# Kernel optimization log

Hardware: AMD Instinct MI355X
Metric: run time of the kernel (lower is better)

The kernel has to match this reference:

```python
import jax, jax.numpy as jnp
import numpy as np

B, N, D, H = 4, 2048, 256, 4
DH = D // H
SS = DH ** -0.25  # sqrt(scale), applied to both qk0 and qk1
EPS = 1e-5


def _split_heads(t):
    # [B, N, D] -> [B, H, N, DH]
    b, n, _ = t.shape
    return t.reshape(b, n, H, DH).transpose(0, 2, 1, 3)


def _merge_heads(t):
    # [B, H, N, DH] -> [B, N, D]
    b, h, n, dh = t.shape
    return t.transpose(0, 2, 1, 3).reshape(b, n, h * dh)


def _layernorm(x, g, b):
    mu = jnp.mean(x, axis=-1, keepdims=True)
    var = jnp.mean(jnp.square(x - mu), axis=-1, keepdims=True)
    return (x - mu) * jax.lax.rsqrt(var + EPS) * g + b


def setup_inputs() -> dict:
    key = jax.random.key(0)
    ks = jax.random.split(key, 16)
    s = 0.02
    return {
        "x0": jax.random.normal(ks[0], (B, N, D), jnp.float32),
        "x1": jax.random.normal(ks[1], (B, N, D), jnp.float32),
        # weights stored as [in, out] (y = x @ W + b), matching torch Linear math
        "Wqk": jax.random.normal(ks[2], (D, D), jnp.float32) * s,
        "bqk": jnp.zeros((D,), jnp.float32),
        "Wv": jax.random.normal(ks[3], (D, D), jnp.float32) * s,
        "bv": jnp.zeros((D,), jnp.float32),
        "Wo": jax.random.normal(ks[4], (D, D), jnp.float32) * s,
        "bo": jnp.zeros((D,), jnp.float32),
        "W1": jax.random.normal(ks[5], (2 * D, 2 * D), jnp.float32) * s,
        "b1": jnp.zeros((2 * D,), jnp.float32),
        "ln_g": jnp.ones((2 * D,), jnp.float32),
        "ln_b": jnp.zeros((2 * D,), jnp.float32),
        "W2": jax.random.normal(ks[6], (2 * D, D), jnp.float32) * s,
        "b2": jnp.zeros((D,), jnp.float32),
    }


def reference(x0, x1, Wqk, bqk, Wv, bv, Wo, bo, W1, b1, ln_g, ln_b, W2, b2):
    qk0 = _split_heads(x0 @ Wqk + bqk) * SS  # [B,H,N,DH]
    qk1 = _split_heads(x1 @ Wqk + bqk) * SS
    v0 = _split_heads(x0 @ Wv + bv)
    v1 = _split_heads(x1 @ Wv + bv)

    # single shared similarity matrix, reused for both softmax directions
    sim = jnp.einsum("bhid,bhjd->bhij", qk0, qk1)  # [B,H,N0,N1]
    attn01 = jax.nn.softmax(sim, axis=-1)                      # rows over j
    attn10 = jax.nn.softmax(jnp.swapaxes(sim, -1, -2), axis=-1)  # rows over i

    m0 = jnp.einsum("bhij,bhjd->bhid", attn01, v1)  # [B,H,N0,DH]
    m1 = jnp.einsum("bhji,bhjd->bhid", jnp.swapaxes(attn10, -1, -2), v0)

    m0 = _merge_heads(m0) @ Wo + bo  # [B,N,D]
    m1 = _merge_heads(m1) @ Wo + bo

    def ffn(x, m):
        h = jnp.concatenate([x, m], axis=-1) @ W1 + b1
        h = jax.nn.gelu(_layernorm(h, ln_g, ln_b), approximate=False)
        return x + h @ W2 + b2

    return ffn(x0, m0), ffn(x1, m1)
```

## Files before the change

### kernel.cpp

```cpp
#include <hip/hip_runtime.h>
#include <hip/hip_bf16.h>
#include <math.h>

#define DEV static __device__ __forceinline__

typedef float f32x4 __attribute__((ext_vector_type(4)));
typedef short s16x8 __attribute__((ext_vector_type(8)));
typedef unsigned short u16;
typedef unsigned int u32;
typedef u32 u32x2 __attribute__((ext_vector_type(2)));
typedef u16 u16x4 __attribute__((ext_vector_type(4)));
typedef u16 u16x8 __attribute__((ext_vector_type(8)));

#define SSCALE 0.35355339059327379f

DEV f32x4 mfma16(s16x8 a, s16x8 b, f32x4 c) {
  return __builtin_amdgcn_mfma_f32_16x16x32_bf16(a, b, c, 0, 0, 0);
}

DEV float bf2f(u16 x) { u32 u = ((u32)x) << 16; float f; __builtin_memcpy(&f, &u, 4); return f; }
DEV u16 f2bf(float x) { __hip_bfloat16 b = __float2bfloat16(x); u16 r; __builtin_memcpy(&r, &b, 2); return r; }

DEV void gload_lds16(const void* g, void* l) {
  __builtin_amdgcn_global_load_lds((const __attribute__((address_space(1))) u32*)g,
                                   (__attribute__((address_space(3))) u32*)l, 16, 0, 0);
}

__global__ __launch_bounds__(256) void k_prep(
    const float* __restrict__ x0, const float* __restrict__ x1,
    const float* __restrict__ Wqk, const float* __restrict__ Wv,
    const float* __restrict__ Wo, const float* __restrict__ W1,
    const float* __restrict__ W2, const float* __restrict__ bo,
    const float* __restrict__ b1,
    u16* __restrict__ btqkv, u16* __restrict__ btF,
    u16* __restrict__ bt2, float* __restrict__ bc, u16* __restrict__ Xb)
{
  const int blk = blockIdx.x, tid = threadIdx.x;
  if (blk < 2048) {
    int idx = blk * 2048 + tid * 8;
    const float* src = (idx < 2097152) ? (x0 + idx) : (x1 + (idx - 2097152));
    f32x4 va = *(const f32x4*)src;
    f32x4 vb = *(const f32x4*)(src + 4);
    u16x8 o;
#pragma unroll
    for (int j = 0; j < 4; ++j) { o[j] = f2bf(va[j]); o[4 + j] = f2bf(vb[j]); }
    *(u16x8*)(Xb + idx) = o;
  } else if (blk < 2144) {
    __shared__ float T[64][65];
    int tb = blk - 2048;
    const float* src; u16* dst; int sld, dld, kr0, c0, drow0;
    if (tb < 16)      { src = Wqk; dst = btqkv; sld = 256; dld = 256; drow0 = 0;
                        kr0 = (tb >> 2) * 64; c0 = (tb & 3) * 64; }
    else if (tb < 32) { tb -= 16; src = Wv; dst = btqkv; sld = 256; dld = 256; drow0 = 256;
                        kr0 = (tb >> 2) * 64; c0 = (tb & 3) * 64; }
    else if (tb < 64) { tb -= 32; src = W1; dst = btF; sld = 512; dld = 512; drow0 = 0;
                        kr0 = (tb >> 3) * 64; c0 = (tb & 7) * 64; }
    else              { tb -= 64; src = W2; dst = bt2; sld = 256; dld = 512; drow0 = 0;
                        kr0 = (tb >> 2) * 64; c0 = (tb & 3) * 64; }
    int r = tid >> 2, cq = (tid & 3) * 16;
#pragma unroll
    for (int q = 0; q < 4; ++q) {
      f32x4 v = *(const f32x4*)(src + (size_t)(kr0 + r) * sld + c0 + cq + q * 4);
#pragma unroll
      for (int e = 0; e < 4; ++e) T[r][cq + q * 4 + e] = v[e];
    }
    __syncthreads();
    int c = tid >> 2, kq = (tid & 3) * 16;
#pragma unroll
    for (int q = 0; q < 2; ++q) {
      u16x8 o;
#pragma unroll
      for (int e = 0; e < 8; ++e) o[e] = f2bf(T[kq + q * 8 + e][c]);
      *(u16x8*)(dst + (size_t)(drow0 + c0 + c) * dld + kr0 + kq + q * 8) = o;
    }
  } else if (blk < 2656) {
    int wb = blk - 2144;
    int i = wb >> 1;
    int n = (wb & 1) * 256 + tid;
    float a0 = 0.f, a1 = 0.f, a2 = 0.f, a3 = 0.f;
    for (int j = 0; j < 256; j += 4) {
      a0 = fmaf(Wo[i * 256 + j],     W1[(size_t)(256 + j) * 512 + n], a0);
      a1 = fmaf(Wo[i * 256 + j + 1], W1[(size_t)(257 + j) * 512 + n], a1);
      a2 = fmaf(Wo[i * 256 + j + 2], W1[(size_t)(258 + j) * 512 + n], a2);
      a3 = fmaf(Wo[i * 256 + j + 3], W1[(size_t)(259 + j) * 512 + n], a3);
    }
    btF[(size_t)n * 512 + 256 + i] = f2bf((a0 + a1) + (a2 + a3));
  } else {
    int n = (blk - 2656) * 256 + tid;
    float acc = b1[n];
    for (int j = 0; j < 256; ++j)
      acc = fmaf(bo[j], W1[(size_t)(256 + j) * 512 + n], acc);
    bc[n] = acc;
  }
}

template <int KD, int K1, int EPI, int BN>
__global__ __launch_bounds__(256, 2) void k_gemm(
    const u16* __restrict__ A1, const u16* __restrict__ A2,
    const u16* __restrict__ Bt,
    const float* __restrict__ bias, const float* __restrict__ bias2,
    const float* __restrict__ res0, const float* __restrict__ res1,
    u16* __restrict__ outb, u16* __restrict__ outb2,
    float* __restrict__ outf, int Ncols)
{
  constexpr int MR = (BN == 128) ? 4 : 2;
  __shared__ char lds[16384 + 2 * BN * 64];
  char* ldsA = lds;
  char* ldsB = lds + 16384;
  const int tid = threadIdx.x;
  const int lane = tid & 63;
  const int w = tid >> 6;
  const int wm = (BN == 128) ? (w >> 1) : w;
  const int wn = (BN == 128) ? (w & 1) : 0;
  const int g = lane >> 4, li = lane & 15;
  const int m0 = blockIdx.x * 128, n0 = blockIdx.y * BN;

  auto stage = [&](int buf, int t) {
    const int k0 = t * 32;
#pragma unroll
    for (int it = 0; it < 2; ++it) {
      int chunk = it * 256 + w * 64 + lane;
      int row = chunk >> 2, c = chunk & 3;
      int kc = k0 + ((c ^ ((row >> 1) & 3)) << 3);
      const u16* src = (kc < K1) ? (A1 + (size_t)(m0 + row) * K1 + kc)
                                 : (A2 + (size_t)(m0 + row) * (KD - K1) + (kc - K1));
      gload_lds16(src, ldsA + buf * 8192 + (it * 256 + w * 64) * 16);
    }
#pragma unroll
    for (int it = 0; it < BN / 64; ++it) {
      int chunk = it * 256 + w * 64 + lane;
      int row = chunk >> 2, c = chunk & 3;
      int kc = k0 + ((c ^ ((row >> 1) & 3)) << 3);
      gload_lds16(Bt + (size_t)(n0 + row) * KD + kc,
                  ldsB + buf * (BN * 64) + (it * 256 + w * 64) * 16);
    }
  };

  f32x4 acc[MR][4] = {};

  stage(0, 0);
  __syncthreads();
  const int NT = KD / 32;
  for (int t = 0; t < NT; ++t) {
    if (t + 1 < NT) stage((t + 1) & 1, t + 1);
    const char* bufA = ldsA + (t & 1) * 8192;
    const char* bufB = ldsB + (t & 1) * (BN * 64);
    s16x8 af[MR], bfr[4];
#pragma unroll
    for (int rt = 0; rt < MR; ++rt) {
      int row = wm * (MR * 16) + rt * 16 + li;
      af[rt] = *(const s16x8*)(bufA + row * 64 + ((g ^ ((row >> 1) & 3)) << 4));
    }
#pragma unroll
    for (int ct = 0; ct < 4; ++ct) {
      int col = wn * 64 + ct * 16 + li;
      bfr[ct] = *(const s16x8*)(bufB + col * 64 + ((g ^ ((col >> 1) & 3)) << 4));
    }
#pragma unroll
    for (int rt = 0; rt < MR; ++rt)
#pragma unroll
      for (int ct = 0; ct < 4; ++ct)
        acc[rt][ct] = mfma16(af[rt], bfr[ct], acc[rt][ct]);
    __syncthreads();
  }

#pragma unroll
  for (int rt = 0; rt < MR; ++rt) {
#pragma unroll
    for (int ct = 0; ct < 4; ++ct) {
      const int growb = m0 + wm * (MR * 16) + rt * 16 + g * 4;
      const int gcol = n0 + wn * 64 + ct * 16 + li;
      if (EPI == 0) {
        const int dir = growb >> 13, bb = (growb >> 11) & 3, n = growb & 2047;
        if (gcol < 256) {
          const int h = gcol >> 6, dh = gcol & 63;
#pragma unroll
          for (int r = 0; r < 4; ++r) {
            float q = (acc[rt][ct][r] + bias[gcol]) * SSCALE;
            outb[((size_t)(dir * 16 + bb * 4 + h) * 2048 + (n + r)) * 64 + dh] = f2bf(q);
          }
        } else {
          const int c2 = gcol - 256, h = c2 >> 6, dh = c2 & 63;
          u16x4 pk;
#pragma unroll
          for (int r = 0; r < 4; ++r) pk[r] = f2bf(acc[rt][ct][r] + bias2[c2]);
          *(u16x4*)(outb2 + ((size_t)(dir * 16 + bb * 4 + h) * 64 + dh) * 2048 + n) = pk;
        }
      } else if (EPI == 1) {
#pragma unroll
        for (int r = 0; r < 4; ++r)
          outb[(size_t)(growb + r) * Ncols + gcol] = f2bf(acc[rt][ct][r] + bias[gcol]);
      } else {
#pragma unroll
        for (int r = 0; r < 4; ++r) {
          int grow = growb + r;
          float x = (grow < 8192) ? res0[(size_t)grow * 256 + gcol]
                                  : res1[(size_t)(grow - 8192) * 256 + gcol];
          outf[(size_t)grow * 256 + gcol] = acc[rt][ct][r] + bias[gcol] + x;
        }
      }
    }
  }
}

__global__ __launch_bounds__(256, 4) void k_attn(
    const u16* __restrict__ qk, const u16* __restrict__ vt, u16* __restrict__ m_all)
{
  __shared__ char Kl[2][8192];
  __shared__ char Vl[2][8192];
  __shared__ char Pl[4][2048];
  const int tid = threadIdx.x, lane = tid & 63, w = tid >> 6;
  const int g = lane >> 4, li = lane & 15;
  const int sw = (blockIdx.x & 7) * 128 + (blockIdx.x >> 3);
  const int qblk = sw & 31;
  const int p = sw >> 5;
  const int dir = p >> 4, bh = p & 15;
  const char* Qg = (const char*)qk + (size_t)p * 262144;
  const char* Kg = (const char*)qk + (size_t)((dir ^ 1) * 16 + bh) * 262144;
  const char* Vg = (const char*)vt + (size_t)((dir ^ 1) * 16 + bh) * 262144;
  const int q0 = qblk * 64 + w * 16;

  s16x8 qf0 = *(const s16x8*)(Qg + (size_t)(q0 + li) * 128 + g * 16);
  s16x8 qf1 = *(const s16x8*)(Qg + (size_t)(q0 + li) * 128 + 64 + g * 16);

  auto stageKV = [&](int buf, int jt) {
#pragma unroll
    for (int it = 0; it < 2; ++it) {
      int chunk = it * 256 + w * 64 + lane;
      int row = chunk >> 3, c = chunk & 7;
      int cc = (c ^ (row & 7)) << 4;
      gload_lds16(Kg + (size_t)(jt * 64 + row) * 128 + cc, &Kl[buf][(it * 256 + w * 64) * 16]);
    }
#pragma unroll
    for (int it = 0; it < 2; ++it) {
      int chunk = it * 256 + w * 64 + lane;
      int row = chunk >> 3, c = chunk & 7;
      int cc = (c ^ (row & 7)) << 4;
      gload_lds16(Vg + (size_t)row * 4096 + jt * 128 + cc, &Vl[buf][(it * 256 + w * 64) * 16]);
    }
  };

  f32x4 acco[4] = {};
  float accl = 0.f;

  stageKV(0, 0);
  __syncthreads();
  for (int jt = 0; jt < 32; ++jt) {
    if (jt + 1 < 32) stageKV((jt + 1) & 1, jt + 1);
    const char* Kb = Kl[jt & 1];
    const char* Vb = Vl[jt & 1];

#pragma unroll
    for (int kt = 0; kt < 4; ++kt) {
      const int krow = kt * 16 + li;
      s16x8 kf0 = *(const s16x8*)(Kb + krow * 128 + ((g ^ (li & 7)) << 4));
      s16x8 kf1 = *(const s16x8*)(Kb + krow * 128 + (((4 + g) ^ (li & 7)) << 4));
      f32x4 s = {0.f, 0.f, 0.f, 0.f};
      s = mfma16(kf0, qf0, s);
      s = mfma16(kf1, qf1, s);
      float p0 = __expf(s[0]), p1 = __expf(s[1]);
      float p2 = __expf(s[2]), p3 = __expf(s[3]);
      accl += (p0 + p1) + (p2 + p3);
      u32x2 pk;
      pk.x = (u32)f2bf(p0) | ((u32)f2bf(p1) << 16);
      pk.y = (u32)f2bf(p2) | ((u32)f2bf(p3) << 16);
      *(u32x2*)(&Pl[w][(li * 128 + kt * 32 + g * 8) ^ ((li & 7) << 4)]) = pk;
    }

#pragma unroll
    for (int ks = 0; ks < 2; ++ks) {
      s16x8 pf = *(const s16x8*)(&Pl[w][(li * 128 + ks * 64 + g * 16) ^ ((li & 7) << 4)]);
#pragma unroll
      for (int dt = 0; dt < 4; ++dt) {
        const int vrow = dt * 16 + li;
        s16x8 vfr = *(const s16x8*)(Vb + vrow * 128 + (((ks * 4 + g) ^ (li & 7)) << 4));
        acco[dt] = mfma16(pf, vfr, acco[dt]);
      }
    }
    __syncthreads();
  }

  accl += __shfl_xor(accl, 16);
  accl += __shfl_xor(accl, 32);
  float inv = 1.0f / accl;
  float invq[4];
#pragma unroll
  for (int r = 0; r < 4; ++r) invq[r] = __shfl(inv, g * 4 + r);

  const int bb = bh >> 2, h = bh & 3;
  const size_t rowb = (size_t)dir * 8192 + (size_t)bb * 2048 + q0 + g * 4;
#pragma unroll
  for (int dt = 0; dt < 4; ++dt)
#pragma unroll
    for (int r = 0; r < 4; ++r)
      m_all[(rowb + r) * 256 + h * 64 + dt * 16 + li] = f2bf(acco[dt][r] * invq[r]);
}

__global__ __launch_bounds__(256) void k_ln_gelu(
    const u16* __restrict__ h, const float* __restrict__ lg,
    const float* __restrict__ lb, u16* __restrict__ o)
{
  int lane = threadIdx.x & 63;
  size_t row = blockIdx.x * 4 + (threadIdx.x >> 6);
  s16x8 v = *(const s16x8*)(h + row * 512 + lane * 8);
  float f[8], s = 0.f, s2 = 0.f;
#pragma unroll
  for (int j = 0; j < 8; ++j) { f[j] = bf2f((u16)v[j]); s += f[j]; s2 += f[j] * f[j]; }
#pragma unroll
  for (int m = 1; m < 64; m <<= 1) { s += __shfl_xor(s, m); s2 += __shfl_xor(s2, m); }
  float mu = s * (1.0f / 512.0f);
  float var = s2 * (1.0f / 512.0f) - mu * mu;
  float rs = rsqrtf(var + 1e-5f);
  s16x8 ov;
#pragma unroll
  for (int j = 0; j < 8; ++j) {
    int c = lane * 8 + j;
    float y = (f[j] - mu) * rs * lg[c] + lb[c];
    float ge = 0.5f * y * (1.0f + erff(y * 0.70710678118654752f));
    ov[j] = (short)f2bf(ge);
  }
  *(s16x8*)(o + row * 512 + lane * 8) = ov;
}

extern "C" void kernel_launch(void* const* d_in, const int* in_sizes, int n_in,
                              void* d_out, int out_size, void* d_ws, size_t ws_size,
                              hipStream_t stream)
{
  const float* x0  = (const float*)d_in[0];
  const float* x1  = (const float*)d_in[1];
  const float* Wqk = (const float*)d_in[2];
  const float* bqk = (const float*)d_in[3];
  const float* Wv  = (const float*)d_in[4];
  const float* bv  = (const float*)d_in[5];
  const float* Wo  = (const float*)d_in[6];
  const float* bo  = (const float*)d_in[7];
  const float* W1  = (const float*)d_in[8];
  const float* b1  = (const float*)d_in[9];
  const float* lg  = (const float*)d_in[10];
  const float* lb  = (const float*)d_in[11];
  const float* W2  = (const float*)d_in[12];
  const float* b2  = (const float*)d_in[13];
  float* out = (float*)d_out;
  char* ws = (char*)d_ws;

  u16*   Xb    = (u16*)(ws + 0);
  u16*   qk    = (u16*)(ws + 8388608);
  u16*   vt    = (u16*)(ws + 16777216);
  u16*   m_all = (u16*)(ws + 25165824);
  u16*   hpre  = (u16*)(ws + 33554432);
  u16*   gact  = (u16*)(ws + 50331648);
  u16*   btqkv = (u16*)(ws + 67108864);
  u16*   btF   = (u16*)(ws + 67371008);
  u16*   bt2   = (u16*)(ws + 67895296);
  float* bc    = (float*)(ws + 68419584);

  k_prep<<<dim3(2658), dim3(256), 0, stream>>>(x0, x1, Wqk, Wv, Wo, W1, W2, bo, b1,
                                               btqkv, btF, bt2, bc, Xb);
  k_gemm<256, 256, 0, 128><<<dim3(128, 4), dim3(256), 0, stream>>>(
      Xb, nullptr, btqkv, bqk, bv, nullptr, nullptr, qk, vt, nullptr, 512);
  k_attn<<<dim3(1024), dim3(256), 0, stream>>>(qk, vt, m_all);
  k_gemm<512, 256, 1, 128><<<dim3(128, 4), dim3(256), 0, stream>>>(
      Xb, m_all, btF, bc, nullptr, nullptr, nullptr, hpre, nullptr, nullptr, 512);
  k_ln_gelu<<<dim3(4096), dim3(256), 0, stream>>>(hpre, lg, lb, gact);
  k_gemm<512, 512, 3, 64><<<dim3(128, 4), dim3(256), 0, stream>>>(
      gact, nullptr, bt2, b2, nullptr, x0, x1, nullptr, nullptr, out, 256);
}
```

Measured before the change: 238.1 us.

## Keep attention probabilities in registers via permlane swap and double query tile per wave

The attention kernel now handles 32 query rows per wave (128 per block) instead of 16, so each K and V fragment loaded from LDS feeds two MFMAs and the grid halves. The shared-memory round trip for the probability tile is removed: K rows are permuted and v_permlane32_swap_b32 rearranges the packed bf16 probabilities directly into the A-operand layout for the PV MFMA. This cuts LDS traffic and per-tile barriers relative to the work done. In exchange it uses more registers (launch bound lowered to 2 blocks per CU) and halves the number of blocks, which reduces occupancy and parallel slack.

```diff
diff --git a/kernel.cpp b/kernel.cpp
--- a/kernel.cpp
+++ b/kernel.cpp
@@ -203,25 +203,29 @@
   }
 }
 
-__global__ __launch_bounds__(256, 4) void k_attn(
+__global__ __launch_bounds__(256, 2) void k_attn(
     const u16* __restrict__ qk, const u16* __restrict__ vt, u16* __restrict__ m_all)
 {
   __shared__ char Kl[2][8192];
   __shared__ char Vl[2][8192];
-  __shared__ char Pl[4][2048];
   const int tid = threadIdx.x, lane = tid & 63, w = tid >> 6;
   const int g = lane >> 4, li = lane & 15;
-  const int sw = (blockIdx.x & 7) * 128 + (blockIdx.x >> 3);
-  const int qblk = sw & 31;
-  const int p = sw >> 5;
+  const int sw = (blockIdx.x & 7) * 64 + (blockIdx.x >> 3);
+  const int qblk = sw & 15;
+  const int p = sw >> 4;
   const int dir = p >> 4, bh = p & 15;
   const char* Qg = (const char*)qk + (size_t)p * 262144;
   const char* Kg = (const char*)qk + (size_t)((dir ^ 1) * 16 + bh) * 262144;
   const char* Vg = (const char*)vt + (size_t)((dir ^ 1) * 16 + bh) * 262144;
-  const int q0 = qblk * 64 + w * 16;
-
-  s16x8 qf0 = *(const s16x8*)(Qg + (size_t)(q0 + li) * 128 + g * 16);
-  s16x8 qf1 = *(const s16x8*)(Qg + (size_t)(q0 + li) * 128 + 64 + g * 16);
+  const int q0 = qblk * 128 + w * 32;
+  const int perm = (li & 3) | ((li & 4) << 1) | ((li & 8) >> 1);
+
+  s16x8 qf[2][2];
+#pragma unroll
+  for (int qt = 0; qt < 2; ++qt)
+#pragma unroll
+    for (int h = 0; h < 2; ++h)
+      qf[qt][h] = *(const s16x8*)(Qg + (size_t)(q0 + qt * 16 + li) * 128 + h * 64 + g * 16);
 
   auto stageKV = [&](int buf, int jt) {
 #pragma unroll
@@ -240,8 +244,8 @@
     }
   };
 
-  f32x4 acco[4] = {};
-  float accl = 0.f;
+  f32x4 acco[2][4] = {};
+  float accl[2] = {0.f, 0.f};
 
   stageKV(0, 0);
   __syncthreads();
@@ -250,50 +254,71 @@
     const char* Kb = Kl[jt & 1];
     const char* Vb = Vl[jt & 1];
 
+    u32 pw[4][2][2];
 #pragma unroll
     for (int kt = 0; kt < 4; ++kt) {
-      const int krow = kt * 16 + li;
-      s16x8 kf0 = *(const s16x8*)(Kb + krow * 128 + ((g ^ (li & 7)) << 4));
-      s16x8 kf1 = *(const s16x8*)(Kb + krow * 128 + (((4 + g) ^ (li & 7)) << 4));
-      f32x4 s = {0.f, 0.f, 0.f, 0.f};
-      s = mfma16(kf0, qf0, s);
-      s = mfma16(kf1, qf1, s);
-      float p0 = __expf(s[0]), p1 = __expf(s[1]);
-      float p2 = __expf(s[2]), p3 = __expf(s[3]);
-      accl += (p0 + p1) + (p2 + p3);
-      u32x2 pk;
-      pk.x = (u32)f2bf(p0) | ((u32)f2bf(p1) << 16);
-      pk.y = (u32)f2bf(p2) | ((u32)f2bf(p3) << 16);
-      *(u32x2*)(&Pl[w][(li * 128 + kt * 32 + g * 8) ^ ((li & 7) << 4)]) = pk;
-    }
-
-#pragma unroll
-    for (int ks = 0; ks < 2; ++ks) {
-      s16x8 pf = *(const s16x8*)(&Pl[w][(li * 128 + ks * 64 + g * 16) ^ ((li & 7) << 4)]);
+      const int krow = kt * 16 + perm;
+      s16x8 kf0 = *(const s16x8*)(Kb + krow * 128 + ((g ^ (krow & 7)) << 4));
+      s16x8 kf1 = *(const s16x8*)(Kb + krow * 128 + (((4 + g) ^ (krow & 7)) << 4));
+#pragma unroll
+      for (int qt = 0; qt < 2; ++qt) {
+        f32x4 s = {0.f, 0.f, 0.f, 0.f};
+        s = mfma16(kf0, qf[qt][0], s);
+        s = mfma16(kf1, qf[qt][1], s);
+        float p0 = __expf(s[0]), p1 = __expf(s[1]);
+        float p2 = __expf(s[2]), p3 = __expf(s[3]);
+        accl[qt] += (p0 + p1) + (p2 + p3);
+        pw[kt][qt][0] = (u32)f2bf(p0) | ((u32)f2bf(p1) << 16);
+        pw[kt][qt][1] = (u32)f2bf(p2) | ((u32)f2bf(p3) << 16);
+      }
+    }
+
+    s16x8 pf[2][2];
+#pragma unroll
+    for (int ks = 0; ks < 2; ++ks)
+#pragma unroll
+      for (int qt = 0; qt < 2; ++qt) {
+        u32 a0 = pw[ks * 2][qt][0], b0 = pw[ks * 2 + 1][qt][0];
+        u32 a1 = pw[ks * 2][qt][1], b1 = pw[ks * 2 + 1][qt][1];
+        asm("v_permlane32_swap_b32 %0, %1" : "+v"(a0), "+v"(b0));
+        asm("v_permlane32_swap_b32 %0, %1" : "+v"(a1), "+v"(b1));
+        u32 words[4] = {a0, a1, b0, b1};
+        __builtin_memcpy(&pf[ks][qt], words, 16);
+      }
+
+#pragma unroll
+    for (int ks = 0; ks < 2; ++ks)
 #pragma unroll
       for (int dt = 0; dt < 4; ++dt) {
         const int vrow = dt * 16 + li;
-        s16x8 vfr = *(const s16x8*)(Vb + vrow * 128 + (((ks * 4 + g) ^ (li & 7)) << 4));
-        acco[dt] = mfma16(pf, vfr, acco[dt]);
+        s16x8 vfr = *(const s16x8*)(Vb + vrow * 128 + (((ks * 4 + g) ^ (vrow & 7)) << 4));
+        acco[0][dt] = mfma16(pf[ks][0], vfr, acco[0][dt]);
+        acco[1][dt] = mfma16(pf[ks][1], vfr, acco[1][dt]);
       }
-    }
     __syncthreads();
   }
 
-  accl += __shfl_xor(accl, 16);
-  accl += __shfl_xor(accl, 32);
-  float inv = 1.0f / accl;
-  float invq[4];
-#pragma unroll
-  for (int r = 0; r < 4; ++r) invq[r] = __shfl(inv, g * 4 + r);
+  float invq[2][4];
+#pragma unroll
+  for (int qt = 0; qt < 2; ++qt) {
+    float v = accl[qt];
+    v += __shfl_xor(v, 16);
+    v += __shfl_xor(v, 32);
+    float inv = 1.0f / v;
+#pragma unroll
+    for (int r = 0; r < 4; ++r) invq[qt][r] = __shfl(inv, g * 4 + r);
+  }
 
   const int bb = bh >> 2, h = bh & 3;
-  const size_t rowb = (size_t)dir * 8192 + (size_t)bb * 2048 + q0 + g * 4;
-#pragma unroll
-  for (int dt = 0; dt < 4; ++dt)
-#pragma unroll
-    for (int r = 0; r < 4; ++r)
-      m_all[(rowb + r) * 256 + h * 64 + dt * 16 + li] = f2bf(acco[dt][r] * invq[r]);
+#pragma unroll
+  for (int qt = 0; qt < 2; ++qt) {
+    const size_t rowb = (size_t)dir * 8192 + (size_t)bb * 2048 + q0 + qt * 16 + g * 4;
+#pragma unroll
+    for (int dt = 0; dt < 4; ++dt)
+#pragma unroll
+      for (int r = 0; r < 4; ++r)
+        m_all[(rowb + r) * 256 + h * 64 + dt * 16 + li] = f2bf(acco[qt][dt][r] * invq[qt][r]);
+  }
 }
 
 __global__ __launch_bounds__(256) void k_ln_gelu(
@@ -358,7 +383,7 @@
                                                btqkv, btF, bt2, bc, Xb);
   k_gemm<256, 256, 0, 128><<<dim3(128, 4), dim3(256), 0, stream>>>(
       Xb, nullptr, btqkv, bqk, bv, nullptr, nullptr, qk, vt, nullptr, 512);
-  k_attn<<<dim3(1024), dim3(256), 0, stream>>>(qk, vt, m_all);
+  k_attn<<<dim3(512), dim3(256), 0, stream>>>(qk, vt, m_all);
   k_gemm<512, 256, 1, 128><<<dim3(128, 4), dim3(256), 0, stream>>>(
       Xb, m_all, btF, bc, nullptr, nullptr, nullptr, hpre, nullptr, nullptr, 512);
   k_ln_gelu<<<dim3(4096), dim3(256), 0, stream>>>(hpre, lg, lb, gact);
```

Result: faster. 230.4 us (-3.2%).
